# Kernel tuning notes

Hardware: AMD Instinct MI355X
Metric: run time of the kernel (lower is better)

The kernel has to match this reference:

```python
import jax, jax.numpy as jnp
import numpy as np

B, S, HID = 4, 2048, 768
NH, DH = 12, 64          # num heads, per-head attention_size
AHS = NH * DH            # all_head_size
EPS = 1e-5


def setup_inputs() -> dict:
    key = jax.random.key(0)
    ks = jax.random.split(key, 12)
    sd = 0.02
    return {
        "hidden_states": jax.random.normal(ks[0], (B, S, HID), jnp.float32),
        "attention_mask": jnp.ones((B, S), jnp.float32),
        "Wq": jax.random.normal(ks[1], (HID, AHS), jnp.float32) * sd,
        "bq": jnp.zeros((AHS,), jnp.float32),
        "Wk": jax.random.normal(ks[2], (HID, AHS), jnp.float32) * sd,
        "bk": jnp.zeros((AHS,), jnp.float32),
        "Wv": jax.random.normal(ks[3], (HID, AHS), jnp.float32) * sd,
        "bv": jnp.zeros((AHS,), jnp.float32),
        "Wo": jax.random.normal(ks[4], (AHS, HID), jnp.float32) * sd,
        "bo": jnp.zeros((HID,), jnp.float32),
        "ln_g": jnp.ones((HID,), jnp.float32),
        "ln_b": jnp.zeros((HID,), jnp.float32),
    }


def reference(hidden_states, attention_mask, Wq, bq, Wk, bk, Wv, bv, Wo, bo, ln_g, ln_b):
    x = hidden_states
    # QKV projections -> (B, S, NH, DH)
    q = (x @ Wq + bq).reshape(B, S, NH, DH)
    k = (x @ Wk + bk).reshape(B, S, NH, DH)
    v = (x @ Wv + bv).reshape(B, S, NH, DH)
    # scaled dot-product scores (B, NH, S, S)
    scores = jnp.einsum("bqhd,bkhd->bhqk", q, k) / jnp.sqrt(jnp.float32(DH))
    # mask: (B, S) -> additive bias on key axis
    scores = scores + ((1.0 - attention_mask) * -10000.0)[:, None, None, :]
    probs = jax.nn.softmax(scores, axis=-1)  # dropout = identity (eval)
    ctx = jnp.einsum("bhqk,bkhd->bqhd", probs, v).reshape(B, S, AHS)
    out = ctx @ Wo + bo  # dropout = identity (eval)
    # residual + LayerNorm
    y = out + x
    mu = jnp.mean(y, axis=-1, keepdims=True)
    var = jnp.mean(jnp.square(y - mu), axis=-1, keepdims=True)
    return (y - mu) * jax.lax.rsqrt(var + EPS) * ln_g + ln_b
```

## Files before the change

kernel.cpp:

```cpp
#include <hip/hip_runtime.h>
#include <cstdint>

typedef __bf16 bf16x8 __attribute__((ext_vector_type(8)));
typedef float f32x4 __attribute__((ext_vector_type(4)));
typedef float f32x16 __attribute__((ext_vector_type(16)));

#define NHEADS 12
#define BATCH 4
#define SEQ 2048
#define HID 768
#define DHEAD 64
#define TOTHEADS 48
#define MROWS 8192
#define LOG2E 1.4426950408889634f

__device__ __forceinline__ ushort f2bf(float f) {
  union { float f; uint32_t u; } v; v.f = f;
  uint32_t u = v.u;
  uint32_t r = (u + 0x7fffu + ((u >> 16) & 1u)) >> 16;
  return (ushort)r;
}

__device__ __forceinline__ float bf2f(ushort u) {
  union { uint32_t u; float f; } v; v.u = (uint32_t)u << 16; return v.f;
}

__device__ __forceinline__ void gload_lds16(const void* g, void* l) {
  __builtin_amdgcn_global_load_lds((const __attribute__((address_space(1))) void*)g,
                                   (__attribute__((address_space(3))) void*)l, 16, 0, 0);
}

__device__ __forceinline__ float xor32_max(float x) {
  float t = x;
  asm("v_permlane32_swap_b32 %0, %1" : "+v"(t), "+v"(x));
  return fmaxf(t, x);
}
__device__ __forceinline__ float xor32_add(float x) {
  float t = x;
  asm("v_permlane32_swap_b32 %0, %1" : "+v"(t), "+v"(x));
  return t + x;
}

__global__ void cvt_x_kernel(const float* __restrict__ x, ushort* __restrict__ xb,
                             const float* __restrict__ mask, ushort* __restrict__ biasArr) {
  int bid = blockIdx.x;
  if (bid < 6144) {
    int i = bid * 256 + threadIdx.x;
    const float4 v = *reinterpret_cast<const float4*>(&x[(size_t)i * 4]);
    ushort4 o;
    o.x = f2bf(v.x); o.y = f2bf(v.y); o.z = f2bf(v.z); o.w = f2bf(v.w);
    *reinterpret_cast<ushort4*>(&xb[(size_t)i * 4]) = o;
  } else {
    int i = (bid - 6144) * 256 + threadIdx.x;
    const float4 mv = *reinterpret_cast<const float4*>(&mask[(size_t)i * 4]);
    ushort4 bv;
    bv.x = f2bf((1.0f - mv.x) * -10000.0f * LOG2E);
    bv.y = f2bf((1.0f - mv.y) * -10000.0f * LOG2E);
    bv.z = f2bf((1.0f - mv.z) * -10000.0f * LOG2E);
    bv.w = f2bf((1.0f - mv.w) * -10000.0f * LOG2E);
    *reinterpret_cast<ushort4*>(&biasArr[(size_t)i * 4]) = bv;
  }
}

__global__ void transpose_all_kernel(const float* __restrict__ W0, const float* __restrict__ W1,
                                     const float* __restrict__ W2, const float* __restrict__ W3,
                                     ushort* __restrict__ wqkvT, ushort* __restrict__ woT) {
  __shared__ float tile[32][33];
  int z = blockIdx.z;
  const float* W = (z == 0) ? W0 : (z == 1) ? W1 : (z == 2) ? W2 : W3;
  ushort* Wt = (z == 3) ? woT : wqkvT + (size_t)z * HID * HID;
  int bx = blockIdx.x * 32;
  int by = blockIdx.y * 32;
  int tx = threadIdx.x, ty = threadIdx.y;
#pragma unroll
  for (int i = 0; i < 32; i += 8)
    tile[ty + i][tx] = W[(size_t)(by + ty + i) * HID + bx + tx];
  __syncthreads();
#pragma unroll
  for (int i = 0; i < 32; i += 8)
    Wt[(size_t)(bx + ty + i) * HID + by + tx] = f2bf(tile[tx][ty + i]);
}

__device__ __forceinline__ void gemm_mainloop(const ushort* __restrict__ A,
                                              const ushort* __restrict__ Bt,
                                              int row0, int col0,
                                              ushort* As, ushort* Bs,
                                              f32x4 (&acc)[4][4], int wv, int lane) {
  const int RW = (wv >> 1) * 64, CW = (wv & 1) * 64;
  const int rr = wv * 16 + (lane >> 2);
  const int cc = (lane & 3) * 8;
  const ushort* A0 = A + (size_t)(row0 + rr) * 768 + cc;
  const ushort* A1 = A + (size_t)(row0 + 64 + rr) * 768 + cc;
  const ushort* B0 = Bt + (size_t)(col0 + rr) * 768 + cc;
  const ushort* B1 = Bt + (size_t)(col0 + 64 + rr) * 768 + cc;
  gload_lds16(A0, As + (wv * 16) * 32);
  gload_lds16(A1, As + (64 + wv * 16) * 32);
  gload_lds16(B0, Bs + (wv * 16) * 32);
  gload_lds16(B1, Bs + (64 + wv * 16) * 32);
  __syncthreads();
  for (int k0 = 0; k0 < 768; k0 += 32) {
    const int buf = (k0 >> 5) & 1;
    if (k0 + 32 < 768) {
      ushort* AsN = As + (buf ^ 1) * (128 * 32);
      ushort* BsN = Bs + (buf ^ 1) * (128 * 32);
      gload_lds16(A0 + k0 + 32, AsN + (wv * 16) * 32);
      gload_lds16(A1 + k0 + 32, AsN + (64 + wv * 16) * 32);
      gload_lds16(B0 + k0 + 32, BsN + (wv * 16) * 32);
      gload_lds16(B1 + k0 + 32, BsN + (64 + wv * 16) * 32);
    }
    const ushort* AsB = As + buf * (128 * 32);
    const ushort* BsB = Bs + buf * (128 * 32);
    bf16x8 a[4], b[4];
#pragma unroll
    for (int m = 0; m < 4; ++m)
      a[m] = *reinterpret_cast<const bf16x8*>(&AsB[(RW + m * 16 + (lane & 15)) * 32 + (lane >> 4) * 8]);
#pragma unroll
    for (int n = 0; n < 4; ++n)
      b[n] = *reinterpret_cast<const bf16x8*>(&BsB[(CW + n * 16 + (lane & 15)) * 32 + (lane >> 4) * 8]);
    __builtin_amdgcn_s_setprio(1);
#pragma unroll
    for (int m = 0; m < 4; ++m)
#pragma unroll
      for (int n = 0; n < 4; ++n)
        acc[m][n] = __builtin_amdgcn_mfma_f32_16x16x32_bf16(a[m], b[n], acc[m][n], 0, 0, 0);
    __builtin_amdgcn_s_setprio(0);
    __syncthreads();
  }
}

__global__ __launch_bounds__(256) void gemm_qkv_kernel(const ushort* __restrict__ A,
                                                       const ushort* __restrict__ Bt,
                                                       const float* __restrict__ bq,
                                                       const float* __restrict__ bk,
                                                       const float* __restrict__ bv,
                                                       ushort* __restrict__ Qo,
                                                       ushort* __restrict__ Ko,
                                                       ushort* __restrict__ Vto) {
  __shared__ ushort As[2 * 128 * 32];
  __shared__ ushort Bs[2 * 128 * 32];
  int tid = threadIdx.x, wv = tid >> 6, lane = tid & 63;
  int row0 = blockIdx.x * 128, col0 = blockIdx.y * 128;
  f32x4 acc[4][4] = {};
  gemm_mainloop(A, Bt, row0, col0, As, Bs, acc, wv, lane);

  const int RW = (wv >> 1) * 64, CW = (wv & 1) * 64;
#pragma unroll
  for (int m = 0; m < 4; ++m)
#pragma unroll
    for (int n = 0; n < 4; ++n) {
      int col = col0 + CW + n * 16 + (lane & 15);
      int t = col / 768, rem = col % 768;
      int hh = rem / 64, d = rem % 64;
      const float* bias = (t == 0) ? bq : ((t == 1) ? bk : bv);
      float bvv = bias[rem];
      int row_base = row0 + RW + m * 16 + (lane >> 4) * 4;
      int bb = row_base >> 11;
      int s0 = row_base & 2047;
      int head = bb * NHEADS + hh;
      if (t == 2) {
        ushort4 vv;
        vv.x = f2bf(acc[m][n][0] + bvv);
        vv.y = f2bf(acc[m][n][1] + bvv);
        vv.z = f2bf(acc[m][n][2] + bvv);
        vv.w = f2bf(acc[m][n][3] + bvv);
        *reinterpret_cast<ushort4*>(&Vto[((size_t)head * DHEAD + d) * SEQ + s0]) = vv;
      } else {
        ushort* dst = (t == 0) ? Qo : Ko;
        float scl = (t == 0) ? (0.125f * LOG2E) : 1.0f;
#pragma unroll
        for (int j = 0; j < 4; ++j)
          dst[((size_t)head * SEQ + s0 + j) * DHEAD + d] = f2bf((acc[m][n][j] + bvv) * scl);
      }
    }
}

__global__ __launch_bounds__(256) void gemm_out_kernel(const ushort* __restrict__ A,
                                                       const ushort* __restrict__ Bt,
                                                       const float* __restrict__ bo,
                                                       ushort* __restrict__ tmpb) {
  __shared__ ushort As[2 * 128 * 32];
  __shared__ ushort Bs[2 * 128 * 32];
  int tid = threadIdx.x, wv = tid >> 6, lane = tid & 63;
  int row0 = blockIdx.x * 128, col0 = blockIdx.y * 128;
  f32x4 acc[4][4] = {};
  gemm_mainloop(A, Bt, row0, col0, As, Bs, acc, wv, lane);

  const int RW = (wv >> 1) * 64, CW = (wv & 1) * 64;
#pragma unroll
  for (int m = 0; m < 4; ++m)
#pragma unroll
    for (int n = 0; n < 4; ++n) {
      int col = col0 + CW + n * 16 + (lane & 15);
      float bvv = bo[col];
      int row_base = row0 + RW + m * 16 + (lane >> 4) * 4;
#pragma unroll
      for (int j = 0; j < 4; ++j)
        tmpb[(size_t)(row_base + j) * HID + col] = f2bf(acc[m][n][j] + bvv);
    }
}

__device__ __forceinline__ void stage_kv(const ushort*& kp0, const ushort*& kp1,
                                         const ushort* vp0, const ushort* vp1, int k0,
                                         ushort* Kd, ushort* Vd, int wb) {
  gload_lds16(kp0, Kd + wb * 64);
  gload_lds16(kp1, Kd + (wb + 8) * 64);
  gload_lds16(vp0 + k0, Vd + wb * 64);
  gload_lds16(vp1 + k0, Vd + (wb + 8) * 64);
  kp0 += 64 * DHEAD; kp1 += 64 * DHEAD;
}

__device__ __forceinline__ void attn_tile(const ushort* __restrict__ KsB,
                                          const ushort* __restrict__ VsB,
                                          const ushort* __restrict__ biasL, int k0,
                                          const bf16x8 (&bq)[4], bool bz,
                                          f32x16 (&accO)[2], float& mrun, float& lrun,
                                          int lo, int hi) {
  f32x16 ps[2];
  if (bz) {
#pragma unroll
    for (int kb = 0; kb < 2; ++kb)
#pragma unroll
      for (int r = 0; r < 16; ++r) ps[kb][r] = 0.f;
  } else {
#pragma unroll
    for (int kb = 0; kb < 2; ++kb)
#pragma unroll
      for (int g = 0; g < 4; ++g) {
        const ushort4 bb = *reinterpret_cast<const ushort4*>(&biasL[k0 + kb * 32 + g * 8 + hi * 4]);
        ps[kb][g * 4 + 0] = bf2f(bb.x); ps[kb][g * 4 + 1] = bf2f(bb.y);
        ps[kb][g * 4 + 2] = bf2f(bb.z); ps[kb][g * 4 + 3] = bf2f(bb.w);
      }
  }
  __builtin_amdgcn_s_setprio(1);
#pragma unroll
  for (int kb = 0; kb < 2; ++kb) {
    int key = kb * 32 + lo;
#pragma unroll
    for (int kd = 0; kd < 4; ++kd) {
      bf16x8 ak = *reinterpret_cast<const bf16x8*>(
          &KsB[key * 64 + ((kd * 16 + hi * 8) ^ ((key & 7) << 3))]);
      ps[kb] = __builtin_amdgcn_mfma_f32_32x32x16_bf16(ak, bq[kd], ps[kb], 0, 0, 0);
    }
  }
  __builtin_amdgcn_s_setprio(0);

  bf16x8 av[2][2][2];
#pragma unroll
  for (int nb = 0; nb < 2; ++nb) {
    int d = nb * 32 + lo;
#pragma unroll
    for (int kb = 0; kb < 2; ++kb)
#pragma unroll
      for (int kk = 0; kk < 2; ++kk)
        av[nb][kb][kk] = *reinterpret_cast<const bf16x8*>(
            &VsB[d * 64 + ((kb * 32 + kk * 16 + hi * 8) ^ ((d & 7) << 3))]);
  }

  float mx[8];
#pragma unroll
  for (int i = 0; i < 8; ++i)
    mx[i] = fmaxf(fmaxf(ps[0][i], ps[0][i + 8]), fmaxf(ps[1][i], ps[1][i + 8]));
  float m01 = fmaxf(fmaxf(mx[0], mx[1]), mx[2]);
  float m23 = fmaxf(fmaxf(mx[3], mx[4]), mx[5]);
  float rm = fmaxf(fmaxf(m01, m23), fmaxf(mx[6], mx[7]));
  rm = xor32_max(rm);

  if (!__all(rm <= mrun + 8.f)) {
    float mnew = fmaxf(mrun, rm);
    float scl = exp2f(mrun - mnew);
    mrun = mnew;
    lrun *= scl;
#pragma unroll
    for (int nb = 0; nb < 2; ++nb)
#pragma unroll
      for (int r = 0; r < 16; ++r) accO[nb][r] *= scl;
  }

#pragma unroll
  for (int kb = 0; kb < 2; ++kb)
#pragma unroll
    for (int r = 0; r < 16; ++r)
      ps[kb][r] = exp2f(ps[kb][r] - mrun);

  float sm[8];
#pragma unroll
  for (int i = 0; i < 8; ++i)
    sm[i] = (ps[0][i] + ps[0][i + 8]) + (ps[1][i] + ps[1][i + 8]);
  float rs = ((sm[0] + sm[1]) + (sm[2] + sm[3])) + ((sm[4] + sm[5]) + (sm[6] + sm[7]));
  rs = xor32_add(rs);
  lrun += rs;

  __builtin_amdgcn_s_setprio(1);
#pragma unroll
  for (int kb = 0; kb < 2; ++kb) {
    uint w[8];
#pragma unroll
    for (int i = 0; i < 8; ++i) {
      float a0 = ps[kb][2 * i], a1 = ps[kb][2 * i + 1];
      asm("v_cvt_pk_bf16_f32 %0, %1, %2" : "=v"(w[i]) : "v"(a0), "v"(a1));
    }
    asm("v_permlane32_swap_b32 %0, %1" : "+v"(w[0]), "+v"(w[2]));
    asm("v_permlane32_swap_b32 %0, %1" : "+v"(w[1]), "+v"(w[3]));
    asm("v_permlane32_swap_b32 %0, %1" : "+v"(w[4]), "+v"(w[6]));
    asm("v_permlane32_swap_b32 %0, %1" : "+v"(w[5]), "+v"(w[7]));
    uint4 u0 = make_uint4(w[0], w[1], w[2], w[3]);
    uint4 u1 = make_uint4(w[4], w[5], w[6], w[7]);
    bf16x8 pa0 = __builtin_bit_cast(bf16x8, u0);
    bf16x8 pa1 = __builtin_bit_cast(bf16x8, u1);
#pragma unroll
    for (int nb = 0; nb < 2; ++nb) {
      accO[nb] = __builtin_amdgcn_mfma_f32_32x32x16_bf16(av[nb][kb][0], pa0, accO[nb], 0, 0, 0);
      accO[nb] = __builtin_amdgcn_mfma_f32_32x32x16_bf16(av[nb][kb][1], pa1, accO[nb], 0, 0, 0);
    }
  }
  __builtin_amdgcn_s_setprio(0);
}

__global__ __launch_bounds__(256, 4) void attn_kernel(const ushort* __restrict__ Q,
                                                      const ushort* __restrict__ Kg,
                                                      const ushort* __restrict__ Vt,
                                                      const ushort* __restrict__ biasArr,
                                                      ushort* __restrict__ ctx) {
  __shared__ ushort Ks[2][64 * 64];
  __shared__ ushort Vs[2][64 * 64];
  __shared__ ushort biasL[SEQ];

  int tid = threadIdx.x, wv = tid >> 6, lane = tid & 63;
  int lo = lane & 31, hi = lane >> 5;

  int bid = blockIdx.x;
  int x = bid & 7, j = bid >> 3;
  int hh = x * 6 + (j >> 4);
  int qt = j & 15;
  int b = hh / NHEADS, h = hh % NHEADS;
  int q0w = qt * 128 + wv * 32;

  const ushort* Qh = Q + (size_t)hh * SEQ * DHEAD;
  const ushort* Kh = Kg + (size_t)hh * SEQ * DHEAD;
  const ushort* Vh = Vt + (size_t)hh * DHEAD * SEQ;
  const ushort* brow = biasArr + (size_t)b * SEQ;

  int r8 = lane >> 3, sc = ((lane & 7) ^ r8) * 8;
  int wb = wv * 16;
  const ushort* kp0 = Kh + (size_t)(wb + r8) * DHEAD + sc;
  const ushort* kp1 = kp0 + (size_t)8 * DHEAD;
  const ushort* vp0 = Vh + (size_t)(wb + r8) * SEQ + sc;
  const ushort* vp1 = vp0 + (size_t)8 * SEQ;

  gload_lds16(brow + wv * 512 + lane * 8, biasL + wv * 512);

  bf16x8 bq[4];
#pragma unroll
  for (int kd = 0; kd < 4; ++kd)
    bq[kd] = *reinterpret_cast<const bf16x8*>(&Qh[(size_t)(q0w + lo) * DHEAD + kd * 16 + hi * 8]);

  f32x16 accO[2] = {};
  float mrun = -1e30f, lrun = 0.f;

  stage_kv(kp0, kp1, vp0, vp1, 0, Ks[0], Vs[0], wb);
  __syncthreads();

  const ushort4* blv = reinterpret_cast<const ushort4*>(biasL);
  ushort4 b0 = blv[tid * 2], b1 = blv[tid * 2 + 1];
  uint anyb = (uint)(b0.x | b0.y | b0.z | b0.w | b1.x | b1.y | b1.z | b1.w);
  bool bz = __syncthreads_and(anyb == 0u) != 0;

  for (int k0 = 0; k0 < SEQ; k0 += 128) {
    stage_kv(kp0, kp1, vp0, vp1, k0 + 64, Ks[1], Vs[1], wb);
    attn_tile(Ks[0], Vs[0], biasL, k0, bq, bz, accO, mrun, lrun, lo, hi);
    __syncthreads();
    if (k0 + 128 < SEQ)
      stage_kv(kp0, kp1, vp0, vp1, k0 + 128, Ks[0], Vs[0], wb);
    attn_tile(Ks[1], Vs[1], biasL, k0 + 64, bq, bz, accO, mrun, lrun, lo, hi);
    __syncthreads();
  }

  float inv = 1.0f / lrun;
  size_t rowbase = ((size_t)(b * SEQ) + q0w + lo) * HID + h * DHEAD;
#pragma unroll
  for (int nb = 0; nb < 2; ++nb)
#pragma unroll
    for (int g = 0; g < 4; ++g) {
      ushort4 o;
      o.x = f2bf(accO[nb][g * 4 + 0] * inv);
      o.y = f2bf(accO[nb][g * 4 + 1] * inv);
      o.z = f2bf(accO[nb][g * 4 + 2] * inv);
      o.w = f2bf(accO[nb][g * 4 + 3] * inv);
      int d = nb * 32 + g * 8 + hi * 4;
      *reinterpret_cast<ushort4*>(&ctx[rowbase + d]) = o;
    }
}

__global__ __launch_bounds__(256) void ln_kernel(const ushort* __restrict__ tmpb,
                                                 const ushort* __restrict__ xb,
                                                 const float* __restrict__ g,
                                                 const float* __restrict__ bta,
                                                 float* __restrict__ out) {
  int wv = threadIdx.x >> 6, lane = threadIdx.x & 63;
  int row = blockIdx.x * 4 + wv;
  const ushort* tr = tmpb + (size_t)row * HID;
  const ushort* xr = xb + (size_t)row * HID;
  float v[12];
  float s = 0.f, ss = 0.f;
#pragma unroll
  for (int i = 0; i < 3; ++i) {
    int c = i * 256 + lane * 4;
    ushort4 tv = *reinterpret_cast<const ushort4*>(&tr[c]);
    ushort4 xv = *reinterpret_cast<const ushort4*>(&xr[c]);
    float a0 = bf2f(tv.x) + bf2f(xv.x);
    float a1 = bf2f(tv.y) + bf2f(xv.y);
    float a2 = bf2f(tv.z) + bf2f(xv.z);
    float a3 = bf2f(tv.w) + bf2f(xv.w);
    v[i * 4 + 0] = a0; v[i * 4 + 1] = a1; v[i * 4 + 2] = a2; v[i * 4 + 3] = a3;
    s += (a0 + a1) + (a2 + a3);
    ss += (a0 * a0 + a1 * a1) + (a2 * a2 + a3 * a3);
  }
#pragma unroll
  for (int msk = 1; msk < 64; msk <<= 1) {
    s += __shfl_xor(s, msk);
    ss += __shfl_xor(ss, msk);
  }
  float mu = s * (1.f / HID);
  float var = ss * (1.f / HID) - mu * mu;
  float inv = rsqrtf(var + 1e-5f);
  float* orow = out + (size_t)row * HID;
#pragma unroll
  for (int i = 0; i < 3; ++i) {
    int c = i * 256 + lane * 4;
    const float4 gv = *reinterpret_cast<const float4*>(&g[c]);
    const float4 bv = *reinterpret_cast<const float4*>(&bta[c]);
    float4 ov;
    ov.x = (v[i * 4 + 0] - mu) * inv * gv.x + bv.x;
    ov.y = (v[i * 4 + 1] - mu) * inv * gv.y + bv.y;
    ov.z = (v[i * 4 + 2] - mu) * inv * gv.z + bv.z;
    ov.w = (v[i * 4 + 3] - mu) * inv * gv.w + bv.w;
    *reinterpret_cast<float4*>(&orow[c]) = ov;
  }
}

extern "C" void kernel_launch(void* const* d_in, const int* in_sizes, int n_in,
                              void* d_out, int out_size, void* d_ws, size_t ws_size,
                              hipStream_t stream) {
  const float* x    = (const float*)d_in[0];
  const float* mask = (const float*)d_in[1];
  const float* Wq   = (const float*)d_in[2];
  const float* bq   = (const float*)d_in[3];
  const float* Wk   = (const float*)d_in[4];
  const float* bk   = (const float*)d_in[5];
  const float* Wv   = (const float*)d_in[6];
  const float* bv   = (const float*)d_in[7];
  const float* Wo   = (const float*)d_in[8];
  const float* bo   = (const float*)d_in[9];
  const float* lng  = (const float*)d_in[10];
  const float* lnb  = (const float*)d_in[11];
  float* out = (float*)d_out;

  char* w = (char*)d_ws;
  size_t o = 0;
  ushort* xb    = (ushort*)(w + o); o += (size_t)MROWS * HID * 2;
  ushort* wqkvT = (ushort*)(w + o); o += (size_t)3 * HID * HID * 2;
  ushort* woT   = (ushort*)(w + o); o += (size_t)HID * HID * 2;
  size_t qb_off = o;
  ushort* Qb    = (ushort*)(w + o); o += (size_t)TOTHEADS * SEQ * DHEAD * 2;
  ushort* Kb    = (ushort*)(w + o); o += (size_t)TOTHEADS * SEQ * DHEAD * 2;
  ushort* Vtb   = (ushort*)(w + o); o += (size_t)TOTHEADS * SEQ * DHEAD * 2;
  ushort* ctx   = (ushort*)(w + o); o += (size_t)MROWS * HID * 2;
  ushort* biasArr = (ushort*)(w + o); o += (size_t)BATCH * SEQ * 2;
  ushort* tmpb  = (ushort*)(w + qb_off);

  cvt_x_kernel<<<6152, 256, 0, stream>>>(x, xb, mask, biasArr);
  dim3 tb(32, 8), tg3(HID / 32, HID / 32, 4);
  transpose_all_kernel<<<tg3, tb, 0, stream>>>(Wq, Wk, Wv, Wo, wqkvT, woT);

  gemm_qkv_kernel<<<dim3(MROWS / 128, 2304 / 128), 256, 0, stream>>>(
      xb, wqkvT, bq, bk, bv, Qb, Kb, Vtb);

  attn_kernel<<<TOTHEADS * 16, 256, 0, stream>>>(Qb, Kb, Vtb, biasArr, ctx);

  gemm_out_kernel<<<dim3(MROWS / 128, HID / 128), 256, 0, stream>>>(ctx, woT, bo, tmpb);

  ln_kernel<<<MROWS / 4, 256, 0, stream>>>(tmpb, xb, lng, lnb, out);
}
```

Measured before the change: 201.6 us.

## Merge prep kernels, narrow out-GEMM tiles, restructure attention QK init and bounds

Merges the input-conversion and weight-transpose kernels into one launch, which removes one kernel launch. Rewrites the output projection GEMM with 128x64 tiles so it launches twice as many blocks (768 instead of 384) and fills more compute units. In attention, the no-mask path now passes a zero constant as the accumulator of the first MFMA instead of zero-filling registers, and setprio is raised earlier. The attention launch-bound occupancy hint drops from 4 to 2, which gives more registers per thread but may allow fewer resident waves.

Measured after the change: 177.3 us. 12.0% less time.

```diff
diff --git a/kernel.cpp b/kernel.cpp
--- a/kernel.cpp
+++ b/kernel.cpp
@@ -41,17 +41,22 @@
   return t + x;
 }
 
-__global__ void cvt_x_kernel(const float* __restrict__ x, ushort* __restrict__ xb,
-                             const float* __restrict__ mask, ushort* __restrict__ biasArr) {
+__global__ void prep_kernel(const float* __restrict__ x, ushort* __restrict__ xb,
+                            const float* __restrict__ mask, ushort* __restrict__ biasArr,
+                            const float* __restrict__ W0, const float* __restrict__ W1,
+                            const float* __restrict__ W2, const float* __restrict__ W3,
+                            ushort* __restrict__ wqkvT, ushort* __restrict__ woT) {
+  __shared__ float tile[32][33];
   int bid = blockIdx.x;
+  int tid = threadIdx.x;
   if (bid < 6144) {
-    int i = bid * 256 + threadIdx.x;
+    int i = bid * 256 + tid;
     const float4 v = *reinterpret_cast<const float4*>(&x[(size_t)i * 4]);
     ushort4 o;
     o.x = f2bf(v.x); o.y = f2bf(v.y); o.z = f2bf(v.z); o.w = f2bf(v.w);
     *reinterpret_cast<ushort4*>(&xb[(size_t)i * 4]) = o;
-  } else {
-    int i = (bid - 6144) * 256 + threadIdx.x;
+  } else if (bid < 6152) {
+    int i = (bid - 6144) * 256 + tid;
     const float4 mv = *reinterpret_cast<const float4*>(&mask[(size_t)i * 4]);
     ushort4 bv;
     bv.x = f2bf((1.0f - mv.x) * -10000.0f * LOG2E);
@@ -59,26 +64,22 @@
     bv.z = f2bf((1.0f - mv.z) * -10000.0f * LOG2E);
     bv.w = f2bf((1.0f - mv.w) * -10000.0f * LOG2E);
     *reinterpret_cast<ushort4*>(&biasArr[(size_t)i * 4]) = bv;
-  }
-}
-
-__global__ void transpose_all_kernel(const float* __restrict__ W0, const float* __restrict__ W1,
-                                     const float* __restrict__ W2, const float* __restrict__ W3,
-                                     ushort* __restrict__ wqkvT, ushort* __restrict__ woT) {
-  __shared__ float tile[32][33];
-  int z = blockIdx.z;
-  const float* W = (z == 0) ? W0 : (z == 1) ? W1 : (z == 2) ? W2 : W3;
-  ushort* Wt = (z == 3) ? woT : wqkvT + (size_t)z * HID * HID;
-  int bx = blockIdx.x * 32;
-  int by = blockIdx.y * 32;
-  int tx = threadIdx.x, ty = threadIdx.y;
-#pragma unroll
-  for (int i = 0; i < 32; i += 8)
-    tile[ty + i][tx] = W[(size_t)(by + ty + i) * HID + bx + tx];
-  __syncthreads();
-#pragma unroll
-  for (int i = 0; i < 32; i += 8)
-    Wt[(size_t)(bx + ty + i) * HID + by + tx] = f2bf(tile[tx][ty + i]);
+  } else {
+    int t = bid - 6152;
+    int z = t / 576, rem = t % 576;
+    const float* W = (z == 0) ? W0 : (z == 1) ? W1 : (z == 2) ? W2 : W3;
+    ushort* Wt = (z == 3) ? woT : wqkvT + (size_t)z * HID * HID;
+    int bx = (rem % 24) * 32;
+    int by = (rem / 24) * 32;
+    int tx = tid & 31, ty = tid >> 5;
+#pragma unroll
+    for (int i = 0; i < 32; i += 8)
+      tile[ty + i][tx] = W[(size_t)(by + ty + i) * HID + bx + tx];
+    __syncthreads();
+#pragma unroll
+    for (int i = 0; i < 32; i += 8)
+      Wt[(size_t)(bx + ty + i) * HID + by + tx] = f2bf(tile[tx][ty + i]);
+  }
 }
 
 __device__ __forceinline__ void gemm_mainloop(const ushort* __restrict__ A,
@@ -179,17 +180,51 @@
                                                        const float* __restrict__ bo,
                                                        ushort* __restrict__ tmpb) {
   __shared__ ushort As[2 * 128 * 32];
-  __shared__ ushort Bs[2 * 128 * 32];
+  __shared__ ushort Bs[2 * 64 * 32];
   int tid = threadIdx.x, wv = tid >> 6, lane = tid & 63;
-  int row0 = blockIdx.x * 128, col0 = blockIdx.y * 128;
-  f32x4 acc[4][4] = {};
-  gemm_mainloop(A, Bt, row0, col0, As, Bs, acc, wv, lane);
-
-  const int RW = (wv >> 1) * 64, CW = (wv & 1) * 64;
+  int row0 = blockIdx.x * 128, col0 = blockIdx.y * 64;
+  const int RW = (wv >> 1) * 64, CW = (wv & 1) * 32;
+  const int rr = wv * 16 + (lane >> 2);
+  const int cc = (lane & 3) * 8;
+  const ushort* A0 = A + (size_t)(row0 + rr) * 768 + cc;
+  const ushort* A1 = A + (size_t)(row0 + 64 + rr) * 768 + cc;
+  const ushort* B0 = Bt + (size_t)(col0 + rr) * 768 + cc;
+  f32x4 acc[4][2] = {};
+  gload_lds16(A0, As + (wv * 16) * 32);
+  gload_lds16(A1, As + (64 + wv * 16) * 32);
+  gload_lds16(B0, Bs + (wv * 16) * 32);
+  __syncthreads();
+  for (int k0 = 0; k0 < 768; k0 += 32) {
+    const int buf = (k0 >> 5) & 1;
+    if (k0 + 32 < 768) {
+      ushort* AsN = As + (buf ^ 1) * (128 * 32);
+      ushort* BsN = Bs + (buf ^ 1) * (64 * 32);
+      gload_lds16(A0 + k0 + 32, AsN + (wv * 16) * 32);
+      gload_lds16(A1 + k0 + 32, AsN + (64 + wv * 16) * 32);
+      gload_lds16(B0 + k0 + 32, BsN + (wv * 16) * 32);
+    }
+    const ushort* AsB = As + buf * (128 * 32);
+    const ushort* BsB = Bs + buf * (64 * 32);
+    bf16x8 a[4], b[2];
+#pragma unroll
+    for (int m = 0; m < 4; ++m)
+      a[m] = *reinterpret_cast<const bf16x8*>(&AsB[(RW + m * 16 + (lane & 15)) * 32 + (lane >> 4) * 8]);
+#pragma unroll
+    for (int n = 0; n < 2; ++n)
+      b[n] = *reinterpret_cast<const bf16x8*>(&BsB[(CW + n * 16 + (lane & 15)) * 32 + (lane >> 4) * 8]);
+    __builtin_amdgcn_s_setprio(1);
+#pragma unroll
+    for (int m = 0; m < 4; ++m)
+#pragma unroll
+      for (int n = 0; n < 2; ++n)
+        acc[m][n] = __builtin_amdgcn_mfma_f32_16x16x32_bf16(a[m], b[n], acc[m][n], 0, 0, 0);
+    __builtin_amdgcn_s_setprio(0);
+    __syncthreads();
+  }
 #pragma unroll
   for (int m = 0; m < 4; ++m)
 #pragma unroll
-    for (int n = 0; n < 4; ++n) {
+    for (int n = 0; n < 2; ++n) {
       int col = col0 + CW + n * 16 + (lane & 15);
       float bvv = bo[col];
       int row_base = row0 + RW + m * 16 + (lane >> 4) * 4;
@@ -212,34 +247,38 @@
 __device__ __forceinline__ void attn_tile(const ushort* __restrict__ KsB,
                                           const ushort* __restrict__ VsB,
                                           const ushort* __restrict__ biasL, int k0,
-                                          const bf16x8 (&bq)[4], bool bz,
+                                          const bf16x8 (&bq)[4], const f32x16& zc, bool bz,
                                           f32x16 (&accO)[2], float& mrun, float& lrun,
                                           int lo, int hi) {
   f32x16 ps[2];
+  __builtin_amdgcn_s_setprio(1);
   if (bz) {
 #pragma unroll
-    for (int kb = 0; kb < 2; ++kb)
-#pragma unroll
-      for (int r = 0; r < 16; ++r) ps[kb][r] = 0.f;
+    for (int kb = 0; kb < 2; ++kb) {
+      int key = kb * 32 + lo;
+#pragma unroll
+      for (int kd = 0; kd < 4; ++kd) {
+        bf16x8 ak = *reinterpret_cast<const bf16x8*>(
+            &KsB[key * 64 + ((kd * 16 + hi * 8) ^ ((key & 7) << 3))]);
+        ps[kb] = __builtin_amdgcn_mfma_f32_32x32x16_bf16(ak, bq[kd], (kd == 0) ? zc : ps[kb], 0, 0, 0);
+      }
+    }
   } else {
 #pragma unroll
-    for (int kb = 0; kb < 2; ++kb)
+    for (int kb = 0; kb < 2; ++kb) {
 #pragma unroll
       for (int g = 0; g < 4; ++g) {
         const ushort4 bb = *reinterpret_cast<const ushort4*>(&biasL[k0 + kb * 32 + g * 8 + hi * 4]);
         ps[kb][g * 4 + 0] = bf2f(bb.x); ps[kb][g * 4 + 1] = bf2f(bb.y);
         ps[kb][g * 4 + 2] = bf2f(bb.z); ps[kb][g * 4 + 3] = bf2f(bb.w);
       }
-  }
-  __builtin_amdgcn_s_setprio(1);
-#pragma unroll
-  for (int kb = 0; kb < 2; ++kb) {
-    int key = kb * 32 + lo;
-#pragma unroll
-    for (int kd = 0; kd < 4; ++kd) {
-      bf16x8 ak = *reinterpret_cast<const bf16x8*>(
-          &KsB[key * 64 + ((kd * 16 + hi * 8) ^ ((key & 7) << 3))]);
-      ps[kb] = __builtin_amdgcn_mfma_f32_32x32x16_bf16(ak, bq[kd], ps[kb], 0, 0, 0);
+      int key = kb * 32 + lo;
+#pragma unroll
+      for (int kd = 0; kd < 4; ++kd) {
+        bf16x8 ak = *reinterpret_cast<const bf16x8*>(
+            &KsB[key * 64 + ((kd * 16 + hi * 8) ^ ((key & 7) << 3))]);
+        ps[kb] = __builtin_amdgcn_mfma_f32_32x32x16_bf16(ak, bq[kd], ps[kb], 0, 0, 0);
+      }
     }
   }
   __builtin_amdgcn_s_setprio(0);
@@ -316,7 +355,7 @@
   __builtin_amdgcn_s_setprio(0);
 }
 
-__global__ __launch_bounds__(256, 4) void attn_kernel(const ushort* __restrict__ Q,
+__global__ __launch_bounds__(256, 2) void attn_kernel(const ushort* __restrict__ Q,
                                                       const ushort* __restrict__ Kg,
                                                       const ushort* __restrict__ Vt,
                                                       const ushort* __restrict__ biasArr,
@@ -355,6 +394,7 @@
     bq[kd] = *reinterpret_cast<const bf16x8*>(&Qh[(size_t)(q0w + lo) * DHEAD + kd * 16 + hi * 8]);
 
   f32x16 accO[2] = {};
+  f32x16 zc = {};
   float mrun = -1e30f, lrun = 0.f;
 
   stage_kv(kp0, kp1, vp0, vp1, 0, Ks[0], Vs[0], wb);
@@ -367,11 +407,11 @@
 
   for (int k0 = 0; k0 < SEQ; k0 += 128) {
     stage_kv(kp0, kp1, vp0, vp1, k0 + 64, Ks[1], Vs[1], wb);
-    attn_tile(Ks[0], Vs[0], biasL, k0, bq, bz, accO, mrun, lrun, lo, hi);
+    attn_tile(Ks[0], Vs[0], biasL, k0, bq, zc, bz, accO, mrun, lrun, lo, hi);
     __syncthreads();
     if (k0 + 128 < SEQ)
       stage_kv(kp0, kp1, vp0, vp1, k0 + 128, Ks[0], Vs[0], wb);
-    attn_tile(Ks[1], Vs[1], biasL, k0 + 64, bq, bz, accO, mrun, lrun, lo, hi);
+    attn_tile(Ks[1], Vs[1], biasL, k0 + 64, bq, zc, bz, accO, mrun, lrun, lo, hi);
     __syncthreads();
   }
 
@@ -468,16 +508,15 @@
   ushort* biasArr = (ushort*)(w + o); o += (size_t)BATCH * SEQ * 2;
   ushort* tmpb  = (ushort*)(w + qb_off);
 
-  cvt_x_kernel<<<6152, 256, 0, stream>>>(x, xb, mask, biasArr);
-  dim3 tb(32, 8), tg3(HID / 32, HID / 32, 4);
-  transpose_all_kernel<<<tg3, tb, 0, stream>>>(Wq, Wk, Wv, Wo, wqkvT, woT);
+  prep_kernel<<<6152 + 4 * 576, 256, 0, stream>>>(x, xb, mask, biasArr,
+                                                  Wq, Wk, Wv, Wo, wqkvT, woT);
 
   gemm_qkv_kernel<<<dim3(MROWS / 128, 2304 / 128), 256, 0, stream>>>(
       xb, wqkvT, bq, bk, bv, Qb, Kb, Vtb);
 
   attn_kernel<<<TOTHEADS * 16, 256, 0, stream>>>(Qb, Kb, Vtb, biasArr, ctx);
 
-  gemm_out_kernel<<<dim3(MROWS / 128, HID / 128), 256, 0, stream>>>(ctx, woT, bo, tmpb);
+  gemm_out_kernel<<<dim3(MROWS / 128, HID / 64), 256, 0, stream>>>(ctx, woT, bo, tmpb);
 
   ln_kernel<<<MROWS / 4, 256, 0, stream>>>(tmpb, xb, lng, lnb, out);
 }
```
